# Kernel optimization log

Hardware: AMD Instinct MI355X
Metric: run time of the kernel (lower is better)

The kernel has to match this reference:

```python
import jax, jax.numpy as jnp
import numpy as np

B, D, T = 16, 256, 4096          # batch, latent_d, latent_t
NQ, K, DC = 8, 1024, 128          # num RVQ layers, codebook size, codebook dim
SAMPLE_IDX = (0, 1, 2, 3)         # deterministic stand-in for weighted np.random.choice


def setup_inputs() -> dict:
    key = jax.random.key(0)
    ks = jax.random.split(key, 6)
    return {
        "diffusion_starts": jax.random.normal(ks[0], (B, D, T), jnp.float32),
        "target_latent_codes": jax.random.randint(ks[1], (B, NQ, T), 0, K),
        "Win": jax.random.normal(ks[2], (NQ, DC, D), jnp.float32) / np.float32(np.sqrt(D)),
        "b_in": jnp.zeros((NQ, DC), jnp.float32),
        "Wout": jax.random.normal(ks[3], (NQ, D, DC), jnp.float32) / np.float32(np.sqrt(DC)),
        "b_out": jnp.zeros((NQ, D), jnp.float32),
        "embed": jax.random.normal(ks[4], (NQ, K, DC), jnp.float32),
    }


def reference(diffusion_starts, target_latent_codes, Win, b_in, Wout, b_out, embed):
    residuals = diffusion_starts  # [B, D, T]
    losses = []
    for i in range(NQ):
        x = residuals.transpose(0, 2, 1)                 # [B, T, D]
        xp = jnp.einsum('btd,cd->btc', x, Win[i]) + b_in[i]   # project_in -> [B, T, DC]
        # Codebook is fully detached in the torch module (quantize path detached,
        # logits path detached), so stop_gradient once here.
        e = jax.lax.stop_gradient(embed[i])              # [K, DC]
        x2 = jnp.sum(xp * xp, axis=-1, keepdims=True)    # [B, T, 1]
        e2 = jnp.sum(e * e, axis=-1)                     # [K]
        sq = x2 - 2.0 * jnp.einsum('btc,kc->btk', xp, e) + e2  # [B, T, K] sum_d (x-e)^2
        ind = jnp.argmin(sq, axis=-1)                    # nearest-neighbor lookup
        quant = e[ind]                                   # [B, T, DC]
        qout = jnp.einsum('btc,dc->btd', quant, Wout[i]) + b_out[i]  # project_out
        residuals = residuals - jax.lax.stop_gradient(qout.transpose(0, 2, 1))
        if i in SAMPLE_IDX:
            logits = -sq / DC                            # mean over latent_d of (x - c)^2, negated
            tgt = target_latent_codes[:, i, :]           # [B, T]
            lse = jax.nn.logsumexp(logits, axis=-1)      # [B, T]
            picked = jnp.take_along_axis(logits, tgt[..., None], axis=-1)[..., 0]
            losses.append(jnp.mean(lse - picked))        # cross_entropy, reduction='mean'
    return jnp.mean(jnp.stack(losses))
```

## Files before the change

### kernel.cpp

```cpp
#include <hip/hip_runtime.h>
#include <math.h>

#define B_   16
#define D_   256
#define T_   4096
#define NQn  8
#define K_   1024
#define DC_  128
#define M_   65536

typedef short bf16x8 __attribute__((ext_vector_type(8)));
typedef float f32x4  __attribute__((ext_vector_type(4)));

static __device__ __forceinline__ unsigned short f2bf(float f) {
    unsigned u = __float_as_uint(f);
    unsigned r = (u + 0x7fffu + ((u >> 16) & 1u)) >> 16;
    return (unsigned short)r;
}

static __device__ __forceinline__ int pk2(float lo, float hi) {
    int r;
    asm("v_cvt_pk_bf16_f32 %0, %1, %2" : "=v"(r) : "v"(lo), "v"(hi));
    return r;
}
static __device__ __forceinline__ int sub2(int x, int t) {
    float xl = __uint_as_float(((unsigned)x) << 16);
    float xh = __uint_as_float(((unsigned)x) & 0xFFFF0000u);
    float tl = __uint_as_float(((unsigned)t) << 16);
    float th = __uint_as_float(((unsigned)t) & 0xFFFF0000u);
    return pk2(xl - tl, xh - th);
}

static __device__ __forceinline__ f32x4 MFMA(bf16x8 a, bf16x8 b, f32x4 c) {
    return __builtin_amdgcn_mfma_f32_16x16x32_bf16(a, b, c, 0, 0, 0);
}

#define EXP2(x) __builtin_amdgcn_exp2f(x)
#define LOG2(x) __builtin_amdgcn_logf(x)

__global__ void final_k(const float* __restrict__ acc, float* __restrict__ out) {
    out[0] = acc[0] * (1.f / 262144.f);
}

__global__ __launch_bounds__(256) void prep_all_k(
    const float* __restrict__ Win, const float* __restrict__ bin,
    const float* __restrict__ emb,
    const float* __restrict__ Wout, const float* __restrict__ bout,
    unsigned short* __restrict__ stream, unsigned short* __restrict__ tab,
    float* __restrict__ gbias, float* __restrict__ accp)
{
    const int bid = blockIdx.x;
    const int tid = threadIdx.x;
    if (bid < 321) {
        if (bid == 320) {
            gbias[4096 + tid]       = bin[tid];
            gbias[4096 + 256 + tid] = bin[256 + tid];
            if (tid == 0) accp[0] = 0.f;
            return;
        }
        int u = bid * 256 + tid;
        int idx = u >> 10;
        int q = idx / 20, r = idx - q * 20;
        int w = u & 1023;
        int lane = w & 63, blk = w >> 6;
        int l15 = lane & 15, lg4 = lane >> 4;
        unsigned short o[8];
        if (r < 4) {
            int c  = 32 * r + 16 * (blk >> 3) + l15;
            int d0 = 32 * (blk & 7) + 8 * lg4;
            const float* s = Win + ((size_t)q * DC_ + c) * D_ + d0;
            #pragma unroll
            for (int j = 0; j < 8; ++j) o[j] = f2bf(s[j]);
        } else {
            int ch = r - 4;
            int code = (ch * 4 + (blk >> 2)) * 16 + l15;
            int s4 = blk & 3;
            const float* s = emb + ((size_t)q * K_ + code) * DC_ + 32 * s4 + 4 * lg4;
            const float ESC = 1.44269504089f / 64.0f;
            #pragma unroll
            for (int j = 0; j < 8; ++j)
                o[j] = f2bf(s[16 * (j >> 2) + (j & 3)] * ESC);
        }
        *(int4*)&stream[(size_t)u * 8] = *(int4*)o;
        return;
    }
    __shared__ float E[16][128];
    const int pb = bid - 321;
    const int iq = pb >> 6;
    const int k0 = (pb & 63) << 4;
    {
        const float* src = emb + ((size_t)iq * K_ + k0) * DC_;
        #pragma unroll
        for (int it = 0; it < 2; ++it) {
            int lin = it * 1024 + tid * 4;
            float4 v = *(const float4*)(src + lin);
            *(float4*)&E[lin >> 7][lin & 127] = v;
        }
    }
    __syncthreads();
    if (tid < 16) {
        float e2 = 0.f;
        for (int c2 = 0; c2 < 128; ++c2) { float e = E[tid][c2]; e2 += e * e; }
        gbias[iq * K_ + k0 + tid] = e2 * (1.44269504089f / 128.f);
    }
    if (iq < 3) {
        const int d = tid;
        float acc[16];
        #pragma unroll
        for (int kk = 0; kk < 16; ++kk) acc[kk] = 0.f;
        const float* wp = Wout + ((size_t)iq * D_ + d) * DC_;
        for (int c2 = 0; c2 < 128; ++c2) {
            float w = wp[c2];
            #pragma unroll
            for (int kk = 0; kk < 16; ++kk) acc[kk] = fmaf(E[kk][c2], w, acc[kk]);
        }
        float bo = bout[iq * D_ + d];
        unsigned short* tq = tab + ((size_t)iq << 18);
        #pragma unroll
        for (int kk = 0; kk < 16; ++kk)
            tq[((size_t)(k0 + kk) << 8) + d] = f2bf(acc[kk] + bo);
    }
}

#define GLDS(SRC, DST) __builtin_amdgcn_global_load_lds( \
    (const __attribute__((address_space(1))) unsigned int*)(SRC), \
    (__attribute__((address_space(3))) unsigned int*)(DST), 16, 0, 0)

#define ITERTOP(BUFP) do { \
    BUFP = LDSM + (cslot << 14); \
    asm volatile("s_waitcnt vmcnt(4)" ::: "memory"); \
    __builtin_amdgcn_s_barrier(); \
    int ss_ = (cslot == 0) ? 2 : cslot - 1; \
    const char* sc_ = sp + (wv << 12) + (lane << 4); \
    char* dc_ = LDSM + (ss_ << 14) + (wv << 12); \
    GLDS(sc_, dc_); GLDS(sc_ + 1024, dc_ + 1024); \
    GLDS(sc_ + 2048, dc_ + 2048); GLDS(sc_ + 3072, dc_ + 3072); \
    sp += 16384; if (sp == send) sp = sbase; \
    cslot = (cslot == 2) ? 0 : cslot + 1; \
    __builtin_amdgcn_sched_barrier(0); \
} while (0)

static __device__ __forceinline__ void mfma_chunk(
    const char* bufp, int lane, const bf16x8 (&xpf)[2][4], f32x4 (&acc)[8])
{
    #pragma unroll
    for (int cfp = 0; cfp < 2; ++cfp)
        #pragma unroll
        for (int cl = 0; cl < 2; ++cl) {
            f32x4 a0 = {0.f, 0.f, 0.f, 0.f}, a1 = a0;
            #pragma unroll
            for (int ss = 0; ss < 4; ++ss) {
                bf16x8 a = *(const bf16x8*)(bufp + ((((cfp * 2 + cl) * 4 + ss) * 64 + lane) << 4));
                a0 = MFMA(a, xpf[0][ss], a0);
                a1 = MFMA(a, xpf[1][ss], a1);
            }
            acc[cfp * 4 + cl * 2 + 0] = a0;
            acc[cfp * 4 + cl * 2 + 1] = a1;
        }
}

template<bool LEAN>
static __device__ __forceinline__ void epi8(
    const f32x4 (&acc)[8], int ch, const float* gq, int lg4,
    float (&lsum)[2], float (&bv)[2])
{
    #pragma unroll
    for (int cfp = 0; cfp < 2; ++cfp)
        #pragma unroll
        for (int cl = 0; cl < 2; ++cl) {
            int cfg = ch * 4 + cfp * 2 + cl;
            float4 gv = *(const float4*)(gq + cfg * 16 + lg4 * 4);
            #pragma unroll
            for (int rf = 0; rf < 2; ++rf) {
                const f32x4& A = acc[cfp * 4 + cl * 2 + rf];
                float e0 = EXP2(A[0] - gv.x);
                float e1 = EXP2(A[1] - gv.y);
                float e2 = EXP2(A[2] - gv.z);
                float e3 = EXP2(A[3] - gv.w);
                if (LEAN) {
                    lsum[rf] += (e0 + e1) + (e2 + e3);
                } else {
                    unsigned cv = (unsigned)cfg;
                    float p0 = __uint_as_float((__float_as_uint(e0) & 0xFFFFFF00u) | cv);
                    float p1 = __uint_as_float(((__float_as_uint(e1) & 0xFFFFFF00u) | cv) | 64u);
                    float p2 = __uint_as_float(((__float_as_uint(e2) & 0xFFFFFF00u) | cv) | 128u);
                    float p3 = __uint_as_float(((__float_as_uint(e3) & 0xFFFFFF00u) | cv) | 192u);
                    lsum[rf] += (p0 + p1) + (p2 + p3);
                    bv[rf] = fmaxf(bv[rf], fmaxf(fmaxf(p0, p1), fmaxf(p2, p3)));
                }
            }
        }
}

template<bool LEAN>
static __device__ __forceinline__ void q_body(
    int q, char* LDSM, const float* gb,
    const char*& sp, const char* sbase, const char* send, int& cslot,
    int wv, int lane, int l15, int lg4,
    bf16x8 (&xb)[2][8], const unsigned short* tab, const char* sq, float& loss)
{
    int tgt[2];
    {
        const int* tl = (const int*)(LDSM + 67584);
        tgt[0] = tl[(wv * 4 + q) * 32 + l15];
        tgt[1] = tl[(wv * 4 + q) * 32 + 16 + l15];
    }

    bf16x8 xpf[2][4];
    #pragma unroll
    for (int S = 0; S < 4; ++S) {
        const char* bufp;
        ITERTOP(bufp);
        f32x4 a00 = {0.f, 0.f, 0.f, 0.f}, a01 = a00, a10 = a00, a11 = a00;
        #pragma unroll
        for (int ss = 0; ss < 8; ++ss) {
            bf16x8 w0 = *(const bf16x8*)(bufp + (((ss) * 64 + lane) << 4));
            bf16x8 w1 = *(const bf16x8*)(bufp + (((8 + ss) * 64 + lane) << 4));
            a00 = MFMA(w0, xb[0][ss], a00);
            a01 = MFMA(w0, xb[1][ss], a01);
            a10 = MFMA(w1, xb[0][ss], a10);
            a11 = MFMA(w1, xb[1][ss], a11);
        }
        float4 b0 = *(const float4*)(gb + 4096 + q * 128 + 32 * S + 4 * lg4);
        float4 b1 = *(const float4*)(gb + 4096 + q * 128 + 32 * S + 16 + 4 * lg4);
        int4 u0, u1;
        u0.x = pk2(a00[0] + b0.x, a00[1] + b0.y);
        u0.y = pk2(a00[2] + b0.z, a00[3] + b0.w);
        u0.z = pk2(a10[0] + b1.x, a10[1] + b1.y);
        u0.w = pk2(a10[2] + b1.z, a10[3] + b1.w);
        xpf[0][S] = *(bf16x8*)&u0;
        u1.x = pk2(a01[0] + b0.x, a01[1] + b0.y);
        u1.y = pk2(a01[2] + b0.z, a01[3] + b0.w);
        u1.z = pk2(a11[0] + b1.x, a11[1] + b1.y);
        u1.w = pk2(a11[2] + b1.z, a11[3] + b1.w);
        xpf[1][S] = *(bf16x8*)&u1;
    }

    const float* gq = gb + (q << 10);
    float lsum[2] = {0.f, 0.f};
    float bv[2]   = {0.f, 0.f};
    int   bi[2]   = {0, 0};
    f32x4 A[8], Bq[8];
    {
        const char* bufp;
        ITERTOP(bufp);
        mfma_chunk(bufp, lane, xpf, A);
    }
    #pragma unroll 1
    for (int t = 0; t < 7; ++t) {
        {
            const char* bufp;
            ITERTOP(bufp);
            mfma_chunk(bufp, lane, xpf, Bq);
            epi8<LEAN>(A, 2 * t, gq, lg4, lsum, bv);
        }
        {
            const char* bufp;
            ITERTOP(bufp);
            mfma_chunk(bufp, lane, xpf, A);
            epi8<LEAN>(Bq, 2 * t + 1, gq, lg4, lsum, bv);
        }
    }
    {
        const char* bufp;
        ITERTOP(bufp);
        mfma_chunk(bufp, lane, xpf, Bq);
        epi8<LEAN>(A, 14, gq, lg4, lsum, bv);
    }
    epi8<LEAN>(Bq, 15, gq, lg4, lsum, bv);

    float pickv[2];
    #pragma unroll
    for (int rf = 0; rf < 2; ++rf) {
        int t = tgt[rf];
        const char* fb = sq + ((4 + (t >> 6)) << 14)
                       + (((((t >> 4) & 3) << 8) + (lg4 << 4) + (t & 15)) << 4);
        bf16x8 f0 = *(const bf16x8*)(fb);
        bf16x8 f1 = *(const bf16x8*)(fb + 1024);
        bf16x8 f2 = *(const bf16x8*)(fb + 2048);
        bf16x8 f3 = *(const bf16x8*)(fb + 3072);
        f32x4 pa = {0.f, 0.f, 0.f, 0.f};
        pa = MFMA(f0, xpf[rf][0], pa);
        pa = MFMA(f1, xpf[rf][1], pa);
        pa = MFMA(f2, xpf[rf][2], pa);
        pa = MFMA(f3, xpf[rf][3], pa);
        int r = l15 & 3;
        float dv = (r == 0) ? pa[0] : ((r == 1) ? pa[1] : ((r == 2) ? pa[2] : pa[3]));
        float gt = gq[t];
        pickv[rf] = (lg4 == (l15 >> 2)) ? (dv - gt) : 0.f;
    }

    #pragma unroll
    for (int rf = 0; rf < 2; ++rf) {
        float pk10 = 0.f;
        if (!LEAN) {
            unsigned pb = __float_as_uint(bv[rf]);
            unsigned code = ((pb & 63u) << 4) | (unsigned)(lg4 << 2) | ((pb >> 6) & 3u);
            pk10 = __uint_as_float((pb & 0xFFFFFC00u) | code);
        }
        #pragma unroll
        for (int off = 16; off <= 32; off <<= 1) {
            lsum[rf]  += __shfl_xor(lsum[rf], off);
            pickv[rf] += __shfl_xor(pickv[rf], off);
            if (!LEAN) pk10 = fmaxf(pk10, __shfl_xor(pk10, off));
        }
        if (!LEAN) bi[rf] = (int)(__float_as_uint(pk10) & 1023u);
        if (lane < 16) loss += LOG2(lsum[rf]) - pickv[rf];
    }

    if (!LEAN) {
        const unsigned short* tq = tab + ((size_t)q << 18);
        #pragma unroll
        for (int rf = 0; rf < 2; ++rf) {
            const unsigned short* trow = tq + ((size_t)bi[rf] << 8) + (lg4 << 3);
            #pragma unroll
            for (int s = 0; s < 8; ++s) {
                int4 tv = *(const int4*)(trow + (s << 5));
                int4 xv = *(int4*)&xb[rf][s];
                int4 ov;
                ov.x = sub2(xv.x, tv.x); ov.y = sub2(xv.y, tv.y);
                ov.z = sub2(xv.z, tv.z); ov.w = sub2(xv.w, tv.w);
                *(int4*)&xb[rf][s] = ov;
            }
        }
    }
}

__global__ __launch_bounds__(256, 2) void rvq_k(
    const float* __restrict__ X,
    const unsigned short* __restrict__ stream,
    const float* __restrict__ gbias,
    const unsigned short* __restrict__ tab,
    const int* __restrict__ tlc,
    float* __restrict__ accp)
{
    __shared__ __align__(16) char LDSM[69632];

    const int tid  = threadIdx.x;
    const int lane = tid & 63;
    const int wv   = tid >> 6;
    const int l15  = lane & 15;
    const int lg4  = lane >> 4;
    const int row_base = blockIdx.x * 128 + wv * 32;

    bf16x8 xb[2][8];
    #pragma unroll
    for (int rf = 0; rf < 2; ++rf) {
        const int row = row_base + rf * 16 + l15;
        const float* xpr = X + ((size_t)(row >> 12) << 20) + (row & (T_ - 1));
        #pragma unroll
        for (int s = 0; s < 8; ++s) {
            float f[8];
            #pragma unroll
            for (int j = 0; j < 8; ++j)
                f[j] = xpr[(size_t)((s << 5) + (lg4 << 3) + j) << 12];
            int4 u;
            u.x = pk2(f[0], f[1]); u.y = pk2(f[2], f[3]);
            u.z = pk2(f[4], f[5]); u.w = pk2(f[6], f[7]);
            xb[rf][s] = *(bf16x8*)&u;
        }
    }

    {
        int* tl = (int*)(LDSM + 67584);
        int q0 = lg4;
        int r0 = row_base + l15, r1 = row_base + 16 + l15;
        int t0 = tlc[(size_t)(r0 >> 12) * (NQn * T_) + q0 * T_ + (r0 & (T_ - 1))];
        int t1 = tlc[(size_t)(r1 >> 12) * (NQn * T_) + q0 * T_ + (r1 & (T_ - 1))];
        tl[(wv * 4 + q0) * 32 + l15] = t0;
        tl[(wv * 4 + q0) * 32 + 16 + l15] = t1;
    }
    __builtin_amdgcn_sched_barrier(0);

    const char* sbase = (const char*)stream;
    const char* send  = sbase + 80 * 16384;
    {
        const char* gs = (const char*)gbias;
        #pragma unroll
        for (int k = 0; k < 4; ++k)
            GLDS(gs + (((k * 4 + wv) * 64 + lane) << 4),
                 LDSM + 49152 + ((k * 4 + wv) << 10));
        if (wv < 2)
            GLDS(gs + 16384 + ((wv * 64 + lane) << 4),
                 LDSM + 49152 + 16384 + (wv << 10));
    }
    {
        const char* s0 = sbase + (wv << 12) + (lane << 4);
        char* d0 = LDSM + (wv << 12);
        GLDS(s0, d0); GLDS(s0 + 1024, d0 + 1024);
        GLDS(s0 + 2048, d0 + 2048); GLDS(s0 + 3072, d0 + 3072);
        const char* s1 = s0 + 16384;
        char* d1 = d0 + 16384;
        GLDS(s1, d1); GLDS(s1 + 1024, d1 + 1024);
        GLDS(s1 + 2048, d1 + 2048); GLDS(s1 + 3072, d1 + 3072);
    }
    const char* sp = sbase + 32768;
    int cslot = 0;
    __syncthreads();

    float loss = 0.f;
    const float* gb = (const float*)(LDSM + 49152);

    #pragma unroll 1
    for (int q = 0; q < 3; ++q)
        q_body<false>(q, LDSM, gb, sp, sbase, send, cslot,
                      wv, lane, l15, lg4, xb, tab,
                      sbase + (size_t)q * 327680, loss);
    q_body<true>(3, LDSM, gb, sp, sbase, send, cslot,
                 wv, lane, l15, lg4, xb, tab,
                 sbase + (size_t)3 * 327680, loss);

    asm volatile("s_waitcnt vmcnt(0)" ::: "memory");
    #pragma unroll
    for (int off = 1; off < 64; off <<= 1) loss += __shfl_xor(loss, off);
    if (lane == 0) atomicAdd(accp, loss * 0.69314718056f);
}

extern "C" void kernel_launch(void* const* d_in, const int* in_sizes, int n_in,
                              void* d_out, int out_size, void* d_ws, size_t ws_size,
                              hipStream_t stream_)
{
    (void)in_sizes; (void)n_in; (void)out_size; (void)ws_size;
    const float* dstart = (const float*)d_in[0];
    const int*   tlc    = (const int*)d_in[1];
    const float* Win    = (const float*)d_in[2];
    const float* bin    = (const float*)d_in[3];
    const float* Wout   = (const float*)d_in[4];
    const float* bout   = (const float*)d_in[5];
    const float* emb    = (const float*)d_in[6];

    char* ws = (char*)d_ws;
    size_t off = 0;
    unsigned short* strm = (unsigned short*)(ws + off); off += (size_t)80 * 16384;
    unsigned short* tab  = (unsigned short*)(ws + off); off += (size_t)3 * K_ * D_ * 2;
    float*          gbias= (float*)(ws + off);          off += (size_t)4608 * 4;
    float*          accp = (float*)(ws + off);          off += 256;

    prep_all_k<<<577, 256, 0, stream_>>>(Win, bin, emb, Wout, bout,
                                         strm, tab, gbias, accp);
    rvq_k<<<512, 256, 0, stream_>>>(dstart, strm, gbias, tab, tlc, accp);
    final_k<<<1, 1, 0, stream_>>>(accp, (float*)d_out);
}
```

Before: 153.5 us.

## Halve rows per wave and switch to double-buffered LDS stream for occupancy

Each wave now handles 16 rows instead of 32, halving accumulator and activation registers, and the grid doubles to 1024 blocks. The LDS codebook/weight stream drops from a triple buffer to a double buffer with a full vmcnt(0) wait, shrinking LDS from about 68KB to 51KB so more blocks fit per CU. The aim is higher occupancy and latency hiding, but it doubles total streaming of weights and codebooks from L2 per output row and removes the prefetch slack of the third buffer.

```diff
diff --git a/kernel.cpp b/kernel.cpp
--- a/kernel.cpp
+++ b/kernel.cpp
@@ -128,68 +128,58 @@
 
 #define ITERTOP(BUFP) do { \
     BUFP = LDSM + (cslot << 14); \
-    asm volatile("s_waitcnt vmcnt(4)" ::: "memory"); \
+    asm volatile("s_waitcnt vmcnt(0)" ::: "memory"); \
     __builtin_amdgcn_s_barrier(); \
-    int ss_ = (cslot == 0) ? 2 : cslot - 1; \
     const char* sc_ = sp + (wv << 12) + (lane << 4); \
-    char* dc_ = LDSM + (ss_ << 14) + (wv << 12); \
+    char* dc_ = LDSM + ((cslot ^ 1) << 14) + (wv << 12); \
     GLDS(sc_, dc_); GLDS(sc_ + 1024, dc_ + 1024); \
     GLDS(sc_ + 2048, dc_ + 2048); GLDS(sc_ + 3072, dc_ + 3072); \
     sp += 16384; if (sp == send) sp = sbase; \
-    cslot = (cslot == 2) ? 0 : cslot + 1; \
+    cslot ^= 1; \
     __builtin_amdgcn_sched_barrier(0); \
 } while (0)
 
 static __device__ __forceinline__ void mfma_chunk(
-    const char* bufp, int lane, const bf16x8 (&xpf)[2][4], f32x4 (&acc)[8])
+    const char* bufp, int lane, const bf16x8 (&xpf)[4], f32x4 (&acc)[4])
 {
     #pragma unroll
-    for (int cfp = 0; cfp < 2; ++cfp)
-        #pragma unroll
-        for (int cl = 0; cl < 2; ++cl) {
-            f32x4 a0 = {0.f, 0.f, 0.f, 0.f}, a1 = a0;
-            #pragma unroll
-            for (int ss = 0; ss < 4; ++ss) {
-                bf16x8 a = *(const bf16x8*)(bufp + ((((cfp * 2 + cl) * 4 + ss) * 64 + lane) << 4));
-                a0 = MFMA(a, xpf[0][ss], a0);
-                a1 = MFMA(a, xpf[1][ss], a1);
-            }
-            acc[cfp * 4 + cl * 2 + 0] = a0;
-            acc[cfp * 4 + cl * 2 + 1] = a1;
-        }
+    for (int cf = 0; cf < 4; ++cf) {
+        f32x4 a0 = {0.f, 0.f, 0.f, 0.f};
+        #pragma unroll
+        for (int ss = 0; ss < 4; ++ss) {
+            bf16x8 a = *(const bf16x8*)(bufp + (((cf * 4 + ss) * 64 + lane) << 4));
+            a0 = MFMA(a, xpf[ss], a0);
+        }
+        acc[cf] = a0;
+    }
 }
 
 template<bool LEAN>
 static __device__ __forceinline__ void epi8(
-    const f32x4 (&acc)[8], int ch, const float* gq, int lg4,
-    float (&lsum)[2], float (&bv)[2])
+    const f32x4 (&acc)[4], int ch, const float* gq, int lg4,
+    float& lsum, float& bv)
 {
     #pragma unroll
-    for (int cfp = 0; cfp < 2; ++cfp)
-        #pragma unroll
-        for (int cl = 0; cl < 2; ++cl) {
-            int cfg = ch * 4 + cfp * 2 + cl;
-            float4 gv = *(const float4*)(gq + cfg * 16 + lg4 * 4);
-            #pragma unroll
-            for (int rf = 0; rf < 2; ++rf) {
-                const f32x4& A = acc[cfp * 4 + cl * 2 + rf];
-                float e0 = EXP2(A[0] - gv.x);
-                float e1 = EXP2(A[1] - gv.y);
-                float e2 = EXP2(A[2] - gv.z);
-                float e3 = EXP2(A[3] - gv.w);
-                if (LEAN) {
-                    lsum[rf] += (e0 + e1) + (e2 + e3);
-                } else {
-                    unsigned cv = (unsigned)cfg;
-                    float p0 = __uint_as_float((__float_as_uint(e0) & 0xFFFFFF00u) | cv);
-                    float p1 = __uint_as_float(((__float_as_uint(e1) & 0xFFFFFF00u) | cv) | 64u);
-                    float p2 = __uint_as_float(((__float_as_uint(e2) & 0xFFFFFF00u) | cv) | 128u);
-                    float p3 = __uint_as_float(((__float_as_uint(e3) & 0xFFFFFF00u) | cv) | 192u);
-                    lsum[rf] += (p0 + p1) + (p2 + p3);
-                    bv[rf] = fmaxf(bv[rf], fmaxf(fmaxf(p0, p1), fmaxf(p2, p3)));
-                }
-            }
-        }
+    for (int cf = 0; cf < 4; ++cf) {
+        int cfg = ch * 4 + cf;
+        float4 gv = *(const float4*)(gq + cfg * 16 + lg4 * 4);
+        const f32x4& A = acc[cf];
+        float e0 = EXP2(A[0] - gv.x);
+        float e1 = EXP2(A[1] - gv.y);
+        float e2 = EXP2(A[2] - gv.z);
+        float e3 = EXP2(A[3] - gv.w);
+        if (LEAN) {
+            lsum += (e0 + e1) + (e2 + e3);
+        } else {
+            unsigned cv = (unsigned)cfg;
+            float p0 = __uint_as_float((__float_as_uint(e0) & 0xFFFFFF00u) | cv);
+            float p1 = __uint_as_float(((__float_as_uint(e1) & 0xFFFFFF00u) | cv) | 64u);
+            float p2 = __uint_as_float(((__float_as_uint(e2) & 0xFFFFFF00u) | cv) | 128u);
+            float p3 = __uint_as_float(((__float_as_uint(e3) & 0xFFFFFF00u) | cv) | 192u);
+            lsum += (p0 + p1) + (p2 + p3);
+            bv = fmaxf(bv, fmaxf(fmaxf(p0, p1), fmaxf(p2, p3)));
+        }
+    }
 }
 
 template<bool LEAN>
@@ -197,50 +187,42 @@
     int q, char* LDSM, const float* gb,
     const char*& sp, const char* sbase, const char* send, int& cslot,
     int wv, int lane, int l15, int lg4,
-    bf16x8 (&xb)[2][8], const unsigned short* tab, const char* sq, float& loss)
-{
-    int tgt[2];
-    {
-        const int* tl = (const int*)(LDSM + 67584);
-        tgt[0] = tl[(wv * 4 + q) * 32 + l15];
-        tgt[1] = tl[(wv * 4 + q) * 32 + 16 + l15];
-    }
-
-    bf16x8 xpf[2][4];
+    bf16x8 (&xb)[8], const unsigned short* tab, const char* sq, float& loss)
+{
+    int tgt;
+    {
+        const int* tl = (const int*)(LDSM + 51200);
+        tgt = tl[(wv * 4 + q) * 16 + l15];
+    }
+
+    bf16x8 xpf[4];
     #pragma unroll
     for (int S = 0; S < 4; ++S) {
         const char* bufp;
         ITERTOP(bufp);
-        f32x4 a00 = {0.f, 0.f, 0.f, 0.f}, a01 = a00, a10 = a00, a11 = a00;
+        float4 b0 = *(const float4*)(gb + 4096 + q * 128 + 32 * S + 4 * lg4);
+        float4 b1 = *(const float4*)(gb + 4096 + q * 128 + 32 * S + 16 + 4 * lg4);
+        f32x4 a00 = {0.f, 0.f, 0.f, 0.f}, a10 = a00;
         #pragma unroll
         for (int ss = 0; ss < 8; ++ss) {
             bf16x8 w0 = *(const bf16x8*)(bufp + (((ss) * 64 + lane) << 4));
             bf16x8 w1 = *(const bf16x8*)(bufp + (((8 + ss) * 64 + lane) << 4));
-            a00 = MFMA(w0, xb[0][ss], a00);
-            a01 = MFMA(w0, xb[1][ss], a01);
-            a10 = MFMA(w1, xb[0][ss], a10);
-            a11 = MFMA(w1, xb[1][ss], a11);
-        }
-        float4 b0 = *(const float4*)(gb + 4096 + q * 128 + 32 * S + 4 * lg4);
-        float4 b1 = *(const float4*)(gb + 4096 + q * 128 + 32 * S + 16 + 4 * lg4);
-        int4 u0, u1;
+            a00 = MFMA(w0, xb[ss], a00);
+            a10 = MFMA(w1, xb[ss], a10);
+        }
+        int4 u0;
         u0.x = pk2(a00[0] + b0.x, a00[1] + b0.y);
         u0.y = pk2(a00[2] + b0.z, a00[3] + b0.w);
         u0.z = pk2(a10[0] + b1.x, a10[1] + b1.y);
         u0.w = pk2(a10[2] + b1.z, a10[3] + b1.w);
-        xpf[0][S] = *(bf16x8*)&u0;
-        u1.x = pk2(a01[0] + b0.x, a01[1] + b0.y);
-        u1.y = pk2(a01[2] + b0.z, a01[3] + b0.w);
-        u1.z = pk2(a11[0] + b1.x, a11[1] + b1.y);
-        u1.w = pk2(a11[2] + b1.z, a11[3] + b1.w);
-        xpf[1][S] = *(bf16x8*)&u1;
+        xpf[S] = *(bf16x8*)&u0;
     }
 
     const float* gq = gb + (q << 10);
-    float lsum[2] = {0.f, 0.f};
-    float bv[2]   = {0.f, 0.f};
-    int   bi[2]   = {0, 0};
-    f32x4 A[8], Bq[8];
+    float lsum = 0.f;
+    float bv   = 0.f;
+    int   bi   = 0;
+    f32x4 A[4], Bq[4];
     {
         const char* bufp;
         ITERTOP(bufp);
@@ -269,10 +251,9 @@
     }
     epi8<LEAN>(Bq, 15, gq, lg4, lsum, bv);
 
-    float pickv[2];
-    #pragma unroll
-    for (int rf = 0; rf < 2; ++rf) {
-        int t = tgt[rf];
+    float pickv;
+    {
+        int t = tgt;
         const char* fb = sq + ((4 + (t >> 6)) << 14)
                        + (((((t >> 4) & 3) << 8) + (lg4 << 4) + (t & 15)) << 4);
         bf16x8 f0 = *(const bf16x8*)(fb);
@@ -280,48 +261,44 @@
         bf16x8 f2 = *(const bf16x8*)(fb + 2048);
         bf16x8 f3 = *(const bf16x8*)(fb + 3072);
         f32x4 pa = {0.f, 0.f, 0.f, 0.f};
-        pa = MFMA(f0, xpf[rf][0], pa);
-        pa = MFMA(f1, xpf[rf][1], pa);
-        pa = MFMA(f2, xpf[rf][2], pa);
-        pa = MFMA(f3, xpf[rf][3], pa);
+        pa = MFMA(f0, xpf[0], pa);
+        pa = MFMA(f1, xpf[1], pa);
+        pa = MFMA(f2, xpf[2], pa);
+        pa = MFMA(f3, xpf[3], pa);
         int r = l15 & 3;
         float dv = (r == 0) ? pa[0] : ((r == 1) ? pa[1] : ((r == 2) ? pa[2] : pa[3]));
         float gt = gq[t];
-        pickv[rf] = (lg4 == (l15 >> 2)) ? (dv - gt) : 0.f;
-    }
-
-    #pragma unroll
-    for (int rf = 0; rf < 2; ++rf) {
+        pickv = (lg4 == (l15 >> 2)) ? (dv - gt) : 0.f;
+    }
+
+    {
         float pk10 = 0.f;
         if (!LEAN) {
-            unsigned pb = __float_as_uint(bv[rf]);
+            unsigned pb = __float_as_uint(bv);
             unsigned code = ((pb & 63u) << 4) | (unsigned)(lg4 << 2) | ((pb >> 6) & 3u);
             pk10 = __uint_as_float((pb & 0xFFFFFC00u) | code);
         }
         #pragma unroll
         for (int off = 16; off <= 32; off <<= 1) {
-            lsum[rf]  += __shfl_xor(lsum[rf], off);
-            pickv[rf] += __shfl_xor(pickv[rf], off);
+            lsum  += __shfl_xor(lsum, off);
+            pickv += __shfl_xor(pickv, off);
             if (!LEAN) pk10 = fmaxf(pk10, __shfl_xor(pk10, off));
         }
-        if (!LEAN) bi[rf] = (int)(__float_as_uint(pk10) & 1023u);
-        if (lane < 16) loss += LOG2(lsum[rf]) - pickv[rf];
+        if (!LEAN) bi = (int)(__float_as_uint(pk10) & 1023u);
+        if (lane < 16) loss += LOG2(lsum) - pickv;
     }
 
     if (!LEAN) {
         const unsigned short* tq = tab + ((size_t)q << 18);
-        #pragma unroll
-        for (int rf = 0; rf < 2; ++rf) {
-            const unsigned short* trow = tq + ((size_t)bi[rf] << 8) + (lg4 << 3);
-            #pragma unroll
-            for (int s = 0; s < 8; ++s) {
-                int4 tv = *(const int4*)(trow + (s << 5));
-                int4 xv = *(int4*)&xb[rf][s];
-                int4 ov;
-                ov.x = sub2(xv.x, tv.x); ov.y = sub2(xv.y, tv.y);
-                ov.z = sub2(xv.z, tv.z); ov.w = sub2(xv.w, tv.w);
-                *(int4*)&xb[rf][s] = ov;
-            }
+        const unsigned short* trow = tq + ((size_t)bi << 8) + (lg4 << 3);
+        #pragma unroll
+        for (int s = 0; s < 8; ++s) {
+            int4 tv = *(const int4*)(trow + (s << 5));
+            int4 xv = *(int4*)&xb[s];
+            int4 ov;
+            ov.x = sub2(xv.x, tv.x); ov.y = sub2(xv.y, tv.y);
+            ov.z = sub2(xv.z, tv.z); ov.w = sub2(xv.w, tv.w);
+            *(int4*)&xb[s] = ov;
         }
     }
 }
@@ -334,19 +311,18 @@
     const int* __restrict__ tlc,
     float* __restrict__ accp)
 {
-    __shared__ __align__(16) char LDSM[69632];
+    __shared__ __align__(16) char LDSM[52224];
 
     const int tid  = threadIdx.x;
     const int lane = tid & 63;
     const int wv   = tid >> 6;
     const int l15  = lane & 15;
     const int lg4  = lane >> 4;
-    const int row_base = blockIdx.x * 128 + wv * 32;
-
-    bf16x8 xb[2][8];
-    #pragma unroll
-    for (int rf = 0; rf < 2; ++rf) {
-        const int row = row_base + rf * 16 + l15;
+    const int row_base = blockIdx.x * 64 + wv * 16;
+
+    bf16x8 xb[8];
+    {
+        const int row = row_base + l15;
         const float* xpr = X + ((size_t)(row >> 12) << 20) + (row & (T_ - 1));
         #pragma unroll
         for (int s = 0; s < 8; ++s) {
@@ -357,18 +333,16 @@
             int4 u;
             u.x = pk2(f[0], f[1]); u.y = pk2(f[2], f[3]);
             u.z = pk2(f[4], f[5]); u.w = pk2(f[6], f[7]);
-            xb[rf][s] = *(bf16x8*)&u;
-        }
-    }
-
-    {
-        int* tl = (int*)(LDSM + 67584);
+            xb[s] = *(bf16x8*)&u;
+        }
+    }
+
+    {
+        int* tl = (int*)(LDSM + 51200);
         int q0 = lg4;
-        int r0 = row_base + l15, r1 = row_base + 16 + l15;
+        int r0 = row_base + l15;
         int t0 = tlc[(size_t)(r0 >> 12) * (NQn * T_) + q0 * T_ + (r0 & (T_ - 1))];
-        int t1 = tlc[(size_t)(r1 >> 12) * (NQn * T_) + q0 * T_ + (r1 & (T_ - 1))];
-        tl[(wv * 4 + q0) * 32 + l15] = t0;
-        tl[(wv * 4 + q0) * 32 + 16 + l15] = t1;
+        tl[(wv * 4 + q0) * 16 + l15] = t0;
     }
     __builtin_amdgcn_sched_barrier(0);
 
@@ -379,27 +353,23 @@
         #pragma unroll
         for (int k = 0; k < 4; ++k)
             GLDS(gs + (((k * 4 + wv) * 64 + lane) << 4),
-                 LDSM + 49152 + ((k * 4 + wv) << 10));
+                 LDSM + 32768 + ((k * 4 + wv) << 10));
         if (wv < 2)
             GLDS(gs + 16384 + ((wv * 64 + lane) << 4),
-                 LDSM + 49152 + 16384 + (wv << 10));
+                 LDSM + 32768 + 16384 + (wv << 10));
     }
     {
         const char* s0 = sbase + (wv << 12) + (lane << 4);
         char* d0 = LDSM + (wv << 12);
         GLDS(s0, d0); GLDS(s0 + 1024, d0 + 1024);
         GLDS(s0 + 2048, d0 + 2048); GLDS(s0 + 3072, d0 + 3072);
-        const char* s1 = s0 + 16384;
-        char* d1 = d0 + 16384;
-        GLDS(s1, d1); GLDS(s1 + 1024, d1 + 1024);
-        GLDS(s1 + 2048, d1 + 2048); GLDS(s1 + 3072, d1 + 3072);
-    }
-    const char* sp = sbase + 32768;
+    }
+    const char* sp = sbase + 16384;
     int cslot = 0;
     __syncthreads();
 
     float loss = 0.f;
-    const float* gb = (const float*)(LDSM + 49152);
+    const float* gb = (const float*)(LDSM + 32768);
 
     #pragma unroll 1
     for (int q = 0; q < 3; ++q)
@@ -438,6 +408,6 @@
 
     prep_all_k<<<577, 256, 0, stream_>>>(Win, bin, emb, Wout, bout,
                                          strm, tab, gbias, accp);
-    rvq_k<<<512, 256, 0, stream_>>>(dstart, strm, gbias, tab, tlc, accp);
+    rvq_k<<<1024, 256, 0, stream_>>>(dstart, strm, gbias, tab, tlc, accp);
     final_k<<<1, 1, 0, stream_>>>(accp, (float*)d_out);
 }
```

Result: slower. 176.6 us (+15.1%).
